# Kernel tuning notes

Measured on AMD Instinct MI355X. Metric: run time of the kernel, lower is better.

The kernel has to match this reference:

```python
import jax, jax.numpy as jnp
import numpy as np
from jax import lax

HUMAN_CONF = 0.7
IOU_TH = 0.5


def setup_inputs() -> dict:
    key = jax.random.key(0)
    k1, k2 = jax.random.split(key)
    B, Q, C = 16, 2048, 2
    return {
        "human_logits": jax.random.normal(k1, (B, Q, C), dtype=jnp.float32),
        "pred_boxes": jax.random.uniform(k2, (B, Q, 4), dtype=jnp.float32),  # cxcywh in [0,1]
        "img_h": 800,
        "img_w": 1333,
    }


def box_cxcywh_to_xyxy(b):
    cx, cy, w, h = b[..., 0], b[..., 1], b[..., 2], b[..., 3]
    return jnp.stack([cx - 0.5 * w, cy - 0.5 * h, cx + 0.5 * w, cy + 0.5 * h], axis=-1)


def pairwise_iou(b):
    # b: [Q,4] xyxy -> iou: [Q,Q]
    area = jnp.clip(b[:, 2] - b[:, 0], 0) * jnp.clip(b[:, 3] - b[:, 1], 0)
    lt = jnp.maximum(b[:, None, :2], b[None, :, :2])
    rb = jnp.minimum(b[:, None, 2:], b[None, :, 2:])
    wh = jnp.clip(rb - lt, 0)
    inter = wh[..., 0] * wh[..., 1]
    union = area[:, None] + area[None, :] - inter
    return inter / jnp.maximum(union, 1e-9)


def nms_keep(boxes, scores, valid, iou_th):
    # Greedy NMS on one image with fixed shapes; returns keep mask [Q].
    Q = scores.shape[0]
    order = jnp.argsort(jnp.where(valid, -scores, jnp.inf))  # valid boxes first, score desc
    b = boxes[order]
    v = valid[order]
    iou = pairwise_iou(b)                       # [Q,Q]
    idx = jnp.arange(Q)
    sup_mat = (iou > iou_th) & (idx[None, :] > idx[:, None])  # i suppresses later j

    def step(supp, i):
        keep_i = v[i] & jnp.logical_not(supp[i])
        supp = supp | (keep_i & sup_mat[i])
        return supp, keep_i

    _, keep_sorted = lax.scan(step, jnp.zeros(Q, bool), idx)
    return jnp.zeros(Q, bool).at[order].set(keep_sorted)


def reference(human_logits, pred_boxes, img_h, img_w):
    prob = jax.nn.softmax(human_logits, axis=-1)          # [B,Q,C]
    scores = prob.max(axis=-1)                            # [B,Q]
    labels = prob.argmax(axis=-1)                         # [B,Q]
    boxes = box_cxcywh_to_xyxy(pred_boxes)                # [B,Q,4]
    scale = jnp.array([img_w, img_h, img_w, img_h], dtype=boxes.dtype)
    boxes = boxes * scale
    valid = (labels == 0) & (scores >= HUMAN_CONF)
    keep = jax.vmap(lambda b, s, v: nms_keep(b, s, v, IOU_TH))(boxes, scores, valid)
    scores_out = jnp.where(keep, scores, 0.0)
    boxes_out = jnp.where(keep[..., None], boxes, 0.0).astype(jnp.int32)
    return scores_out, boxes_out, keep
```

## Files before the change

kernel.cpp:

```cpp
#include <hip/hip_runtime.h>
#include <math.h>


#define QN    2048
#define NS    1024
#define MATW  17408
#define MAGIC 0x5ca1ab1eu

__device__ __forceinline__ int rb32(int wb) { return 64 * wb * (33 - wb); }

__device__ __forceinline__ unsigned long long shfl_xor_u64(unsigned long long x, int m) {
    int lo = __shfl_xor((int)(unsigned)(x & 0xffffffffull), m, 64);
    int hi = __shfl_xor((int)(unsigned)(x >> 32), m, 64);
    return ((unsigned long long)(unsigned)hi << 32) | (unsigned)lo;
}

__device__ __forceinline__ unsigned long long score_key(float2 l, int q, bool* valid_out) {
    float mx = fmaxf(l.x, l.y), mn = fminf(l.x, l.y);
    float e = expf(mn - mx);
    float score = 1.0f / (1.0f + e);
    bool valid = (l.x >= l.y) && (score >= 0.7f);
    *valid_out = valid;
    unsigned sbits = valid ? __float_as_uint(score) : 0u;
    return ((unsigned long long)(~sbits) << 32) | (unsigned)q;
}

__global__ __launch_bounds__(1024) void kfused(
    const float* __restrict__ logits, const float* __restrict__ pboxes,
    const int* __restrict__ img_h_p, const int* __restrict__ img_w_p,
    unsigned* __restrict__ wflag, unsigned* __restrict__ wmat,
    float* __restrict__ out, int B)
{
    __shared__ __align__(16) char smem[32904];
    unsigned long long* skey = (unsigned long long*)smem;
    float* sx1 = (float*)(smem + 8192);
    float* sy1 = (float*)(smem + 12288);
    float* sx2 = (float*)(smem + 16384);
    float* sy2 = (float*)(smem + 20480);
    float* sar = (float*)(smem + 24576);
    unsigned short* sidxl = (unsigned short*)(smem + 28672);
    unsigned char* keepq = (unsigned char*)(smem + 30720);
    unsigned* skm = (unsigned*)(smem + 32768);
    int* sMp = (int*)(smem + 32896);

    const int blk = blockIdx.x;
    const int b = blk % B, slice = blk / B;
    const int tid = threadIdx.x, lane = tid & 63, wave = tid >> 6;
    const float sw = (float)(*img_w_p), sh = (float)(*img_h_p);

    if (tid == 0) *sMp = 0;
    keepq[tid] = 0; keepq[tid + 1024] = 0;
    if (tid < 32) skm[tid] = 0;
    __syncthreads();

    const unsigned long long lmask_lt = (1ull << lane) - 1ull;
#pragma unroll
    for (int qq = 0; qq < 2; ++qq) {
        int q = tid + qq * 1024;
        float2 l = ((const float2*)logits)[b * QN + q];
        bool valid;
        unsigned long long key = score_key(l, q, &valid);
        unsigned long long mb = __ballot(valid);
        int base = 0;
        if (lane == 0 && mb) base = atomicAdd(sMp, __popcll(mb));
        base = __shfl(base, 0, 64);
        if (valid) {
            int slot = base + __popcll(mb & lmask_lt);
            if (slot < NS) skey[slot] = key;
        }
    }
    __syncthreads();
    const int M = *sMp;

    if (M <= NS) {
        unsigned long long v = (tid < M) ? skey[tid] : ~0ull;
        __syncthreads();
#pragma unroll
        for (int k = 2; k <= 64; k <<= 1) {
            bool dir = ((tid & k) == 0);
#pragma unroll
            for (int j = k >> 1; j > 0; j >>= 1) {
                unsigned long long o = shfl_xor_u64(v, j);
                bool takeMin = (dir == ((tid & j) == 0));
                v = ((v < o) == takeMin) ? v : o;
            }
        }
        for (int k = 128; k <= NS; k <<= 1) {
            bool dir = ((tid & k) == 0);
            for (int j = k >> 1; j >= 64; j >>= 1) {
                skey[tid] = v;
                __syncthreads();
                unsigned long long o = skey[tid ^ j];
                bool takeMin = (dir == ((tid & j) == 0));
                v = ((v < o) == takeMin) ? v : o;
                __syncthreads();
            }
#pragma unroll
            for (int j = 32; j > 0; j >>= 1) {
                unsigned long long o = shfl_xor_u64(v, j);
                bool takeMin = (dir == ((tid & j) == 0));
                v = ((v < o) == takeMin) ? v : o;
            }
        }
        int qi = (int)((unsigned)v & 0xffffu);
        sidxl[tid] = (unsigned short)qi;
        float x1 = 0.f, y1 = 0.f, x2 = 0.f, y2 = 0.f, ar = 0.f;
        if (tid < M) {
            float4 pb = ((const float4*)pboxes)[b * QN + qi];
            x1 = (pb.x - 0.5f * pb.z) * sw;
            y1 = (pb.y - 0.5f * pb.w) * sh;
            x2 = (pb.x + 0.5f * pb.z) * sw;
            y2 = (pb.y + 0.5f * pb.w) * sh;
            ar = fmaxf(x2 - x1, 0.f) * fmaxf(y2 - y1, 0.f);
        }
        sx1[tid] = x1; sy1[tid] = y1; sx2[tid] = x2; sy2[tid] = y2; sar[tid] = ar;
        __syncthreads();

        unsigned* mat = wmat + (long)b * MATW;
        const int NG = (M + 3) >> 2;
        const int W64 = (M + 63) >> 6;
        for (int gi = slice * 16 + wave; gi < NG; gi += 128) {
            const int g = gi << 2;
            const int nr = min(4, M - g);
            const int wb = g >> 6;
            const int rl = 32 - 2 * wb;
            float ax1[4], ay1[4], ax2[4], ay2[4], aar[4];
            int rbase[4];
#pragma unroll
            for (int r = 0; r < 4; ++r) {
                int i = g + min(r, nr - 1);
                ax1[r] = sx1[i]; ay1[r] = sy1[i];
                ax2[r] = sx2[i]; ay2[r] = sy2[i]; aar[r] = sar[i];
                rbase[r] = rb32(wb) + ((g + r) & 63) * rl;
            }
            for (int w = wb; w < W64; ++w) {
                int j = (w << 6) | lane;
                float bx1 = sx1[j], by1 = sy1[j], bx2 = sx2[j], by2 = sy2[j], bar = sar[j];
#pragma unroll
                for (int r = 0; r < 4; ++r) {
                    float ltx = fmaxf(ax1[r], bx1), lty = fmaxf(ay1[r], by1);
                    float rbx = fminf(ax2[r], bx2), rby = fminf(ay2[r], by2);
                    float wx = fmaxf(rbx - ltx, 0.f), wy = fmaxf(rby - lty, 0.f);
                    float inter = wx * wy;
                    float uni = aar[r] + bar - inter;
                    float iou = inter / fmaxf(uni, 1e-9f);
                    bool sup = (iou > 0.5f) && (j > g + r);
                    unsigned long long bal = __ballot(sup);
                    if (lane == 0 && r < nr)
                        __hip_atomic_store(
                            (unsigned long long*)(mat + rbase[r] + 2 * (w - wb)), bal,
                            __ATOMIC_RELAXED, __HIP_MEMORY_SCOPE_AGENT);
                }
            }
        }
        __syncthreads();
        if (tid == 0)
            __hip_atomic_store(&wflag[b * 8 + slice], MAGIC,
                               __ATOMIC_RELEASE, __HIP_MEMORY_SCOPE_AGENT);
        if (slice != 0) return;

        if (wave == 0) {
            const unsigned* fp = &wflag[b * 8 + (lane & 7)];
            for (;;) {
                unsigned f = (lane < 8)
                    ? __hip_atomic_load(fp, __ATOMIC_RELAXED, __HIP_MEMORY_SCOPE_AGENT)
                    : MAGIC;
                if (__all(f == MAGIC)) break;
                __builtin_amdgcn_s_sleep(2);
            }
            (void)__hip_atomic_load(&wflag[b * 8], __ATOMIC_ACQUIRE,
                                    __HIP_MEMORY_SCOPE_AGENT);

            const unsigned* gm = wmat + (long)b * MATW;
            unsigned rem = 0;
            const int Ms = __builtin_amdgcn_readfirstlane(M);
            const int C = (Ms + 31) >> 5;
            unsigned rcur[32], rnxt[32];
            if (C > 0) {
                int Lc = min(tid, 31);
#pragma unroll
                for (int t = 0; t < 32; ++t) rcur[t] = gm[Lc + t * 32];
            }
            for (int c = 0; c < C; ++c) {
                if (c + 1 < C) {
                    int cn = c + 1, wbn = cn >> 1, rln = 32 - 2 * wbn;
                    int Lcn = min(max(tid, 2 * wbn), 31);
                    int rb0n = rb32(wbn) + ((cn & 1) << 5) * rln + (Lcn - 2 * wbn);
#pragma unroll
                    for (int t = 0; t < 32; ++t) rnxt[t] = gm[rb0n + t * rln];
                }
                unsigned rw = (unsigned)__builtin_amdgcn_readlane((int)rem, c);
                unsigned keepmask = 0;
                int lim = min(32, Ms - (c << 5));
#pragma unroll
                for (int t = 0; t < 32; ++t) {
                    if (t < lim && !((rw >> t) & 1u)) {
                        keepmask |= (1u << t);
                        rem |= rcur[t];
                        rw |= (unsigned)__builtin_amdgcn_readlane((int)rcur[t], c);
                    }
                }
                if (tid == 0) skm[c] = keepmask;
                if (c + 1 < C) {
#pragma unroll
                    for (int t = 0; t < 32; ++t) rcur[t] = rnxt[t];
                }
            }
        }
        __syncthreads();
        for (int s = tid; s < M; s += 1024)
            if ((skm[s >> 5] >> (s & 31)) & 1u) keepq[sidxl[s]] = 1;
        __syncthreads();
    } else {
        if (slice != 0) return;
        unsigned long long* skeyF = (unsigned long long*)smem;
        unsigned char* ssupp = (unsigned char*)(smem + 16384);
        for (int q = tid; q < QN; q += 1024) {
            float2 l = ((const float2*)logits)[b * QN + q];
            bool valid;
            skeyF[q] = score_key(l, q, &valid);
        }
        __syncthreads();
        for (int k = 2; k <= QN; k <<= 1)
            for (int j = k >> 1; j > 0; j >>= 1) {
                int i = ((tid & ~(j - 1)) << 1) | (tid & (j - 1));
                int p = i | j;
                bool up = ((i & k) == 0);
                unsigned long long a = skeyF[i], c2 = skeyF[p];
                if ((a > c2) == up) { skeyF[i] = c2; skeyF[p] = a; }
                __syncthreads();
            }
        for (int s = tid; s < M; s += 1024) ssupp[s] = 0;
        __syncthreads();
        for (int i = 0; i < M; ++i) {
            __syncthreads();
            if (ssupp[i]) continue;
            int ia = (unsigned short)(unsigned)skeyF[i];
            float4 pa = ((const float4*)pboxes)[b * QN + ia];
            float ax1 = (pa.x - 0.5f * pa.z) * sw, ay1 = (pa.y - 0.5f * pa.w) * sh;
            float ax2 = (pa.x + 0.5f * pa.z) * sw, ay2 = (pa.y + 0.5f * pa.w) * sh;
            float areaA = fmaxf(ax2 - ax1, 0.f) * fmaxf(ay2 - ay1, 0.f);
            for (int jj = i + 1 + tid; jj < M; jj += 1024) {
                int jb = (unsigned short)(unsigned)skeyF[jj];
                float4 pq = ((const float4*)pboxes)[b * QN + jb];
                float bx1 = (pq.x - 0.5f * pq.z) * sw, by1 = (pq.y - 0.5f * pq.w) * sh;
                float bx2 = (pq.x + 0.5f * pq.z) * sw, by2 = (pq.y + 0.5f * pq.w) * sh;
                float ltx = fmaxf(ax1, bx1), lty = fmaxf(ay1, by1);
                float rbx = fminf(ax2, bx2), rby = fminf(ay2, by2);
                float wx = fmaxf(rbx - ltx, 0.f), wy = fmaxf(rby - lty, 0.f);
                float inter = wx * wy;
                float areaB = fmaxf(bx2 - bx1, 0.f) * fmaxf(by2 - by1, 0.f);
                float uni = areaA + areaB - inter;
                if (inter / fmaxf(uni, 1e-9f) > 0.5f) ssupp[jj] = 1;
            }
        }
        __syncthreads();
        for (int s = tid; s < M; s += 1024)
            if (!ssupp[s]) keepq[(unsigned short)(unsigned)skeyF[s]] = 1;
        __syncthreads();
    }

    const long BQ = (long)B * QN;
#pragma unroll
    for (int qq = 0; qq < 2; ++qq) {
        int q = tid + qq * 1024;
        int base = b * QN + q;
        float2 l = ((const float2*)logits)[base];
        float e = expf(fminf(l.x, l.y) - fmaxf(l.x, l.y));
        float score = 1.0f / (1.0f + e);
        float4 pb = ((const float4*)pboxes)[base];
        float x1 = (pb.x - 0.5f * pb.z) * sw, y1 = (pb.y - 0.5f * pb.w) * sh;
        float x2 = (pb.x + 0.5f * pb.z) * sw, y2 = (pb.y + 0.5f * pb.w) * sh;
        int kp = keepq[q];
        out[base] = kp ? score : 0.f;
        out[BQ * 5 + base] = kp ? 1.f : 0.f;
        float4 ob;
        ob.x = kp ? truncf(x1) : 0.f;
        ob.y = kp ? truncf(y1) : 0.f;
        ob.z = kp ? truncf(x2) : 0.f;
        ob.w = kp ? truncf(y2) : 0.f;
        ((float4*)(out + BQ))[base] = ob;
    }
}

extern "C" void kernel_launch(void* const* d_in, const int* in_sizes, int n_in,
                              void* d_out, int out_size, void* d_ws, size_t ws_size,
                              hipStream_t stream) {
    const float* logits = (const float*)d_in[0];
    const float* pboxes = (const float*)d_in[1];
    const int*   img_h  = (const int*)d_in[2];
    const int*   img_w  = (const int*)d_in[3];
    float* out = (float*)d_out;
    const int B = in_sizes[0] / (QN * 2);

    char* ws = (char*)d_ws;
    unsigned* wflag = (unsigned*)(ws + 0);
    unsigned* wmat  = (unsigned*)(ws + 1024);

    kfused<<<dim3(B * 8), dim3(1024), 0, stream>>>(logits, pboxes, img_h, img_w,
                                                   wflag, wmat, out, B);
}
```

Measured before the change: 102.9 us.

## Pipeline NMS scan with per-group flags; slice 0 scans instead of building matrix

Slice 0 no longer computes any suppression-matrix rows. Each of the 7 other slices publishes a per-row-group ready flag, so slice 0's scanning wave waits only for the chunk it needs next instead of for every slice to finish. Slice 0 also prefetches logits and boxes for the output stage while it waits, and the matrix loads become atomic relaxed loads. This overlaps matrix construction with the sequential greedy scan, but it gives up one eighth of the matrix-building workers. It also adds flag polling per chunk, and because flags are never reset between calls it relies on the MAGIC value staying correct across calls.

```diff
diff --git a/kernel.cpp b/kernel.cpp
--- a/kernel.cpp
+++ b/kernel.cpp
@@ -28,7 +28,7 @@
 __global__ __launch_bounds__(1024) void kfused(
     const float* __restrict__ logits, const float* __restrict__ pboxes,
     const int* __restrict__ img_h_p, const int* __restrict__ img_w_p,
-    unsigned* __restrict__ wflag, unsigned* __restrict__ wmat,
+    unsigned* __restrict__ wgflag, unsigned* __restrict__ wmat,
     float* __restrict__ out, int B)
 {
     __shared__ __align__(16) char smem[32904];
@@ -49,8 +49,6 @@
     const float sw = (float)(*img_w_p), sh = (float)(*img_h_p);
 
     if (tid == 0) *sMp = 0;
-    keepq[tid] = 0; keepq[tid + 1024] = 0;
-    if (tid < 32) skm[tid] = 0;
     __syncthreads();
 
     const unsigned long long lmask_lt = (1ull << lane) - 1ull;
@@ -103,91 +101,113 @@
             }
         }
         int qi = (int)((unsigned)v & 0xffffu);
+        const int NG = (M + 3) >> 2;
+
+        if (slice != 0) {
+            float x1 = 0.f, y1 = 0.f, x2 = 0.f, y2 = 0.f, ar = 0.f;
+            if (tid < M) {
+                float4 pb = ((const float4*)pboxes)[b * QN + qi];
+                x1 = (pb.x - 0.5f * pb.z) * sw;
+                y1 = (pb.y - 0.5f * pb.w) * sh;
+                x2 = (pb.x + 0.5f * pb.z) * sw;
+                y2 = (pb.y + 0.5f * pb.w) * sh;
+                ar = fmaxf(x2 - x1, 0.f) * fmaxf(y2 - y1, 0.f);
+            }
+            sx1[tid] = x1; sy1[tid] = y1; sx2[tid] = x2; sy2[tid] = y2; sar[tid] = ar;
+            __syncthreads();
+
+            unsigned* mat = wmat + (long)b * MATW;
+            const int W64 = (M + 63) >> 6;
+            const int W = (slice - 1) * 16 + wave;
+            for (int gi = W; gi < NG; gi += 112) {
+                const int g = gi << 2;
+                const int nr = min(4, M - g);
+                const int wb = g >> 6;
+                const int rl = 32 - 2 * wb;
+                float ax1[4], ay1[4], ax2[4], ay2[4], aar[4];
+                int rbase[4];
+#pragma unroll
+                for (int r = 0; r < 4; ++r) {
+                    int i = g + min(r, nr - 1);
+                    ax1[r] = sx1[i]; ay1[r] = sy1[i];
+                    ax2[r] = sx2[i]; ay2[r] = sy2[i]; aar[r] = sar[i];
+                    rbase[r] = rb32(wb) + ((g + r) & 63) * rl;
+                }
+                for (int w = wb; w < W64; ++w) {
+                    int j = (w << 6) | lane;
+                    float bx1 = sx1[j], by1 = sy1[j], bx2 = sx2[j], by2 = sy2[j], bar = sar[j];
+#pragma unroll
+                    for (int r = 0; r < 4; ++r) {
+                        float ltx = fmaxf(ax1[r], bx1), lty = fmaxf(ay1[r], by1);
+                        float rbx = fminf(ax2[r], bx2), rby = fminf(ay2[r], by2);
+                        float wx = fmaxf(rbx - ltx, 0.f), wy = fmaxf(rby - lty, 0.f);
+                        float inter = wx * wy;
+                        float uni = aar[r] + bar - inter;
+                        float iou = inter / fmaxf(uni, 1e-9f);
+                        bool sup = (iou > 0.5f) && (j > g + r);
+                        unsigned long long bal = __ballot(sup);
+                        if (lane == 0 && r < nr)
+                            __hip_atomic_store(
+                                (unsigned long long*)(mat + rbase[r] + 2 * (w - wb)), bal,
+                                __ATOMIC_RELAXED, __HIP_MEMORY_SCOPE_AGENT);
+                    }
+                }
+                if (lane == 0)
+                    __hip_atomic_store(&wgflag[b * 256 + gi], MAGIC,
+                                       __ATOMIC_RELEASE, __HIP_MEMORY_SCOPE_AGENT);
+            }
+            return;
+        }
+
         sidxl[tid] = (unsigned short)qi;
-        float x1 = 0.f, y1 = 0.f, x2 = 0.f, y2 = 0.f, ar = 0.f;
-        if (tid < M) {
-            float4 pb = ((const float4*)pboxes)[b * QN + qi];
-            x1 = (pb.x - 0.5f * pb.z) * sw;
-            y1 = (pb.y - 0.5f * pb.w) * sh;
-            x2 = (pb.x + 0.5f * pb.z) * sw;
-            y2 = (pb.y + 0.5f * pb.w) * sh;
-            ar = fmaxf(x2 - x1, 0.f) * fmaxf(y2 - y1, 0.f);
-        }
-        sx1[tid] = x1; sy1[tid] = y1; sx2[tid] = x2; sy2[tid] = y2; sar[tid] = ar;
-        __syncthreads();
-
-        unsigned* mat = wmat + (long)b * MATW;
-        const int NG = (M + 3) >> 2;
-        const int W64 = (M + 63) >> 6;
-        for (int gi = slice * 16 + wave; gi < NG; gi += 128) {
-            const int g = gi << 2;
-            const int nr = min(4, M - g);
-            const int wb = g >> 6;
-            const int rl = 32 - 2 * wb;
-            float ax1[4], ay1[4], ax2[4], ay2[4], aar[4];
-            int rbase[4];
-#pragma unroll
-            for (int r = 0; r < 4; ++r) {
-                int i = g + min(r, nr - 1);
-                ax1[r] = sx1[i]; ay1[r] = sy1[i];
-                ax2[r] = sx2[i]; ay2[r] = sy2[i]; aar[r] = sar[i];
-                rbase[r] = rb32(wb) + ((g + r) & 63) * rl;
-            }
-            for (int w = wb; w < W64; ++w) {
-                int j = (w << 6) | lane;
-                float bx1 = sx1[j], by1 = sy1[j], bx2 = sx2[j], by2 = sy2[j], bar = sar[j];
-#pragma unroll
-                for (int r = 0; r < 4; ++r) {
-                    float ltx = fmaxf(ax1[r], bx1), lty = fmaxf(ay1[r], by1);
-                    float rbx = fminf(ax2[r], bx2), rby = fminf(ay2[r], by2);
-                    float wx = fmaxf(rbx - ltx, 0.f), wy = fmaxf(rby - lty, 0.f);
-                    float inter = wx * wy;
-                    float uni = aar[r] + bar - inter;
-                    float iou = inter / fmaxf(uni, 1e-9f);
-                    bool sup = (iou > 0.5f) && (j > g + r);
-                    unsigned long long bal = __ballot(sup);
-                    if (lane == 0 && r < nr)
-                        __hip_atomic_store(
-                            (unsigned long long*)(mat + rbase[r] + 2 * (w - wb)), bal,
-                            __ATOMIC_RELAXED, __HIP_MEMORY_SCOPE_AGENT);
-                }
-            }
-        }
-        __syncthreads();
-        if (tid == 0)
-            __hip_atomic_store(&wflag[b * 8 + slice], MAGIC,
-                               __ATOMIC_RELEASE, __HIP_MEMORY_SCOPE_AGENT);
-        if (slice != 0) return;
+        keepq[tid] = 0; keepq[tid + 1024] = 0;
+        if (tid < 32) skm[tid] = 0;
+
+        float2 l2a = ((const float2*)logits)[b * QN + tid];
+        float2 l2b = ((const float2*)logits)[b * QN + tid + 1024];
+        float4 p4a = ((const float4*)pboxes)[b * QN + tid];
+        float4 p4b = ((const float4*)pboxes)[b * QN + tid + 1024];
 
         if (wave == 0) {
-            const unsigned* fp = &wflag[b * 8 + (lane & 7)];
-            for (;;) {
-                unsigned f = (lane < 8)
-                    ? __hip_atomic_load(fp, __ATOMIC_RELAXED, __HIP_MEMORY_SCOPE_AGENT)
-                    : MAGIC;
-                if (__all(f == MAGIC)) break;
-                __builtin_amdgcn_s_sleep(2);
-            }
-            (void)__hip_atomic_load(&wflag[b * 8], __ATOMIC_ACQUIRE,
-                                    __HIP_MEMORY_SCOPE_AGENT);
-
             const unsigned* gm = wmat + (long)b * MATW;
             unsigned rem = 0;
             const int Ms = __builtin_amdgcn_readfirstlane(M);
             const int C = (Ms + 31) >> 5;
+            const int NGs = (Ms + 3) >> 2;
             unsigned rcur[32], rnxt[32];
+
+#define WAIT_CHUNK(cc)                                                                 \
+            {                                                                          \
+                int gbase = b * 256 + 8 * (cc);                                        \
+                int gcnt = min(8, NGs - 8 * (cc));                                     \
+                for (;;) {                                                             \
+                    unsigned f = (lane < gcnt)                                         \
+                        ? __hip_atomic_load(&wgflag[gbase + lane], __ATOMIC_RELAXED,   \
+                                            __HIP_MEMORY_SCOPE_AGENT)                  \
+                        : MAGIC;                                                       \
+                    if (__all(f == MAGIC)) break;                                      \
+                    __builtin_amdgcn_s_sleep(1);                                       \
+                }                                                                      \
+            }
+
             if (C > 0) {
+                WAIT_CHUNK(0);
                 int Lc = min(tid, 31);
 #pragma unroll
-                for (int t = 0; t < 32; ++t) rcur[t] = gm[Lc + t * 32];
+                for (int t = 0; t < 32; ++t)
+                    rcur[t] = __hip_atomic_load(gm + Lc + t * 32, __ATOMIC_RELAXED,
+                                                __HIP_MEMORY_SCOPE_AGENT);
             }
             for (int c = 0; c < C; ++c) {
                 if (c + 1 < C) {
+                    WAIT_CHUNK(c + 1);
                     int cn = c + 1, wbn = cn >> 1, rln = 32 - 2 * wbn;
                     int Lcn = min(max(tid, 2 * wbn), 31);
                     int rb0n = rb32(wbn) + ((cn & 1) << 5) * rln + (Lcn - 2 * wbn);
 #pragma unroll
-                    for (int t = 0; t < 32; ++t) rnxt[t] = gm[rb0n + t * rln];
+                    for (int t = 0; t < 32; ++t)
+                        rnxt[t] = __hip_atomic_load(gm + rb0n + t * rln, __ATOMIC_RELAXED,
+                                                    __HIP_MEMORY_SCOPE_AGENT);
                 }
                 unsigned rw = (unsigned)__builtin_amdgcn_readlane((int)rem, c);
                 unsigned keepmask = 0;
@@ -206,15 +226,39 @@
                     for (int t = 0; t < 32; ++t) rcur[t] = rnxt[t];
                 }
             }
+#undef WAIT_CHUNK
         }
         __syncthreads();
         for (int s = tid; s < M; s += 1024)
             if ((skm[s >> 5] >> (s & 31)) & 1u) keepq[sidxl[s]] = 1;
         __syncthreads();
+
+        const long BQ = (long)B * QN;
+#pragma unroll
+        for (int qq = 0; qq < 2; ++qq) {
+            int q = tid + qq * 1024;
+            int base = b * QN + q;
+            float2 l = qq ? l2b : l2a;
+            float4 pb = qq ? p4b : p4a;
+            float e = expf(fminf(l.x, l.y) - fmaxf(l.x, l.y));
+            float score = 1.0f / (1.0f + e);
+            float x1 = (pb.x - 0.5f * pb.z) * sw, y1 = (pb.y - 0.5f * pb.w) * sh;
+            float x2 = (pb.x + 0.5f * pb.z) * sw, y2 = (pb.y + 0.5f * pb.w) * sh;
+            int kp = keepq[q];
+            out[base] = kp ? score : 0.f;
+            out[BQ * 5 + base] = kp ? 1.f : 0.f;
+            float4 ob;
+            ob.x = kp ? truncf(x1) : 0.f;
+            ob.y = kp ? truncf(y1) : 0.f;
+            ob.z = kp ? truncf(x2) : 0.f;
+            ob.w = kp ? truncf(y2) : 0.f;
+            ((float4*)(out + BQ))[base] = ob;
+        }
     } else {
         if (slice != 0) return;
         unsigned long long* skeyF = (unsigned long long*)smem;
         unsigned char* ssupp = (unsigned char*)(smem + 16384);
+        keepq[tid] = 0; keepq[tid + 1024] = 0;
         for (int q = tid; q < QN; q += 1024) {
             float2 l = ((const float2*)logits)[b * QN + q];
             bool valid;
@@ -258,28 +302,28 @@
         for (int s = tid; s < M; s += 1024)
             if (!ssupp[s]) keepq[(unsigned short)(unsigned)skeyF[s]] = 1;
         __syncthreads();
-    }
-
-    const long BQ = (long)B * QN;
-#pragma unroll
-    for (int qq = 0; qq < 2; ++qq) {
-        int q = tid + qq * 1024;
-        int base = b * QN + q;
-        float2 l = ((const float2*)logits)[base];
-        float e = expf(fminf(l.x, l.y) - fmaxf(l.x, l.y));
-        float score = 1.0f / (1.0f + e);
-        float4 pb = ((const float4*)pboxes)[base];
-        float x1 = (pb.x - 0.5f * pb.z) * sw, y1 = (pb.y - 0.5f * pb.w) * sh;
-        float x2 = (pb.x + 0.5f * pb.z) * sw, y2 = (pb.y + 0.5f * pb.w) * sh;
-        int kp = keepq[q];
-        out[base] = kp ? score : 0.f;
-        out[BQ * 5 + base] = kp ? 1.f : 0.f;
-        float4 ob;
-        ob.x = kp ? truncf(x1) : 0.f;
-        ob.y = kp ? truncf(y1) : 0.f;
-        ob.z = kp ? truncf(x2) : 0.f;
-        ob.w = kp ? truncf(y2) : 0.f;
-        ((float4*)(out + BQ))[base] = ob;
+
+        const long BQ = (long)B * QN;
+#pragma unroll
+        for (int qq = 0; qq < 2; ++qq) {
+            int q = tid + qq * 1024;
+            int base = b * QN + q;
+            float2 l = ((const float2*)logits)[base];
+            float e = expf(fminf(l.x, l.y) - fmaxf(l.x, l.y));
+            float score = 1.0f / (1.0f + e);
+            float4 pb = ((const float4*)pboxes)[base];
+            float x1 = (pb.x - 0.5f * pb.z) * sw, y1 = (pb.y - 0.5f * pb.w) * sh;
+            float x2 = (pb.x + 0.5f * pb.z) * sw, y2 = (pb.y + 0.5f * pb.w) * sh;
+            int kp = keepq[q];
+            out[base] = kp ? score : 0.f;
+            out[BQ * 5 + base] = kp ? 1.f : 0.f;
+            float4 ob;
+            ob.x = kp ? truncf(x1) : 0.f;
+            ob.y = kp ? truncf(y1) : 0.f;
+            ob.z = kp ? truncf(x2) : 0.f;
+            ob.w = kp ? truncf(y2) : 0.f;
+            ((float4*)(out + BQ))[base] = ob;
+        }
     }
 }
 
@@ -294,9 +338,9 @@
     const int B = in_sizes[0] / (QN * 2);
 
     char* ws = (char*)d_ws;
-    unsigned* wflag = (unsigned*)(ws + 0);
-    unsigned* wmat  = (unsigned*)(ws + 1024);
+    unsigned* wgflag = (unsigned*)(ws + 0);
+    unsigned* wmat   = (unsigned*)(ws + 16384);
 
     kfused<<<dim3(B * 8), dim3(1024), 0, stream>>>(logits, pboxes, img_h, img_w,
-                                                   wflag, wmat, out, B);
+                                                   wgflag, wmat, out, B);
 }
```

After: 113.8 us. 10.6% more time.

## Offload IoU matrix to worker slices; master prefetches outputs inputs during wait

Applied to the files above, without the earlier changes.

Slice 0 no longer computes any part of the suppression bitmask. The IoU work is spread over slices 1-7 and the flag wait covers only those seven. While slice 0 waits, it clears its shared buffers and prefetches the logits and boxes it will need for the output write, so those loads overlap the wait. The trade-off is that the remaining slices each carry more IoU groups, which could lengthen the critical path if slice 0's own share was what hid the latency.

```diff
diff --git a/kernel.cpp b/kernel.cpp
--- a/kernel.cpp
+++ b/kernel.cpp
@@ -49,8 +49,6 @@
     const float sw = (float)(*img_w_p), sh = (float)(*img_h_p);
 
     if (tid == 0) *sMp = 0;
-    keepq[tid] = 0; keepq[tid + 1024] = 0;
-    if (tid < 32) skm[tid] = 0;
     __syncthreads();
 
     const unsigned long long lmask_lt = (1ull << lane) - 1ull;
@@ -103,72 +101,83 @@
             }
         }
         int qi = (int)((unsigned)v & 0xffffu);
+        const int NG = (M + 3) >> 2;
+
+        if (slice != 0) {
+            float x1 = 0.f, y1 = 0.f, x2 = 0.f, y2 = 0.f, ar = 0.f;
+            if (tid < M) {
+                float4 pb = ((const float4*)pboxes)[b * QN + qi];
+                x1 = (pb.x - 0.5f * pb.z) * sw;
+                y1 = (pb.y - 0.5f * pb.w) * sh;
+                x2 = (pb.x + 0.5f * pb.z) * sw;
+                y2 = (pb.y + 0.5f * pb.w) * sh;
+                ar = fmaxf(x2 - x1, 0.f) * fmaxf(y2 - y1, 0.f);
+            }
+            sx1[tid] = x1; sy1[tid] = y1; sx2[tid] = x2; sy2[tid] = y2; sar[tid] = ar;
+            __syncthreads();
+
+            unsigned* mat = wmat + (long)b * MATW;
+            const int W64 = (M + 63) >> 6;
+            for (int gi = (slice - 1) * 16 + wave; gi < NG; gi += 112) {
+                const int g = gi << 2;
+                const int nr = min(4, M - g);
+                const int wb = g >> 6;
+                const int rl = 32 - 2 * wb;
+                float ax1[4], ay1[4], ax2[4], ay2[4], aar[4];
+                int rbase[4];
+#pragma unroll
+                for (int r = 0; r < 4; ++r) {
+                    int i = g + min(r, nr - 1);
+                    ax1[r] = sx1[i]; ay1[r] = sy1[i];
+                    ax2[r] = sx2[i]; ay2[r] = sy2[i]; aar[r] = sar[i];
+                    rbase[r] = rb32(wb) + ((g + r) & 63) * rl;
+                }
+                for (int w = wb; w < W64; ++w) {
+                    int j = (w << 6) | lane;
+                    float bx1 = sx1[j], by1 = sy1[j], bx2 = sx2[j], by2 = sy2[j], bar = sar[j];
+#pragma unroll
+                    for (int r = 0; r < 4; ++r) {
+                        float ltx = fmaxf(ax1[r], bx1), lty = fmaxf(ay1[r], by1);
+                        float rbx = fminf(ax2[r], bx2), rby = fminf(ay2[r], by2);
+                        float wx = fmaxf(rbx - ltx, 0.f), wy = fmaxf(rby - lty, 0.f);
+                        float inter = wx * wy;
+                        float uni = aar[r] + bar - inter;
+                        float iou = inter / fmaxf(uni, 1e-9f);
+                        bool sup = (iou > 0.5f) && (j > g + r);
+                        unsigned long long bal = __ballot(sup);
+                        if (lane == 0 && r < nr)
+                            __hip_atomic_store(
+                                (unsigned long long*)(mat + rbase[r] + 2 * (w - wb)), bal,
+                                __ATOMIC_RELAXED, __HIP_MEMORY_SCOPE_AGENT);
+                    }
+                }
+            }
+            __syncthreads();
+            if (tid == 0)
+                __hip_atomic_store(&wflag[b * 8 + slice], MAGIC,
+                                   __ATOMIC_RELEASE, __HIP_MEMORY_SCOPE_AGENT);
+            return;
+        }
+
         sidxl[tid] = (unsigned short)qi;
-        float x1 = 0.f, y1 = 0.f, x2 = 0.f, y2 = 0.f, ar = 0.f;
-        if (tid < M) {
-            float4 pb = ((const float4*)pboxes)[b * QN + qi];
-            x1 = (pb.x - 0.5f * pb.z) * sw;
-            y1 = (pb.y - 0.5f * pb.w) * sh;
-            x2 = (pb.x + 0.5f * pb.z) * sw;
-            y2 = (pb.y + 0.5f * pb.w) * sh;
-            ar = fmaxf(x2 - x1, 0.f) * fmaxf(y2 - y1, 0.f);
-        }
-        sx1[tid] = x1; sy1[tid] = y1; sx2[tid] = x2; sy2[tid] = y2; sar[tid] = ar;
-        __syncthreads();
-
-        unsigned* mat = wmat + (long)b * MATW;
-        const int NG = (M + 3) >> 2;
-        const int W64 = (M + 63) >> 6;
-        for (int gi = slice * 16 + wave; gi < NG; gi += 128) {
-            const int g = gi << 2;
-            const int nr = min(4, M - g);
-            const int wb = g >> 6;
-            const int rl = 32 - 2 * wb;
-            float ax1[4], ay1[4], ax2[4], ay2[4], aar[4];
-            int rbase[4];
-#pragma unroll
-            for (int r = 0; r < 4; ++r) {
-                int i = g + min(r, nr - 1);
-                ax1[r] = sx1[i]; ay1[r] = sy1[i];
-                ax2[r] = sx2[i]; ay2[r] = sy2[i]; aar[r] = sar[i];
-                rbase[r] = rb32(wb) + ((g + r) & 63) * rl;
-            }
-            for (int w = wb; w < W64; ++w) {
-                int j = (w << 6) | lane;
-                float bx1 = sx1[j], by1 = sy1[j], bx2 = sx2[j], by2 = sy2[j], bar = sar[j];
-#pragma unroll
-                for (int r = 0; r < 4; ++r) {
-                    float ltx = fmaxf(ax1[r], bx1), lty = fmaxf(ay1[r], by1);
-                    float rbx = fminf(ax2[r], bx2), rby = fminf(ay2[r], by2);
-                    float wx = fmaxf(rbx - ltx, 0.f), wy = fmaxf(rby - lty, 0.f);
-                    float inter = wx * wy;
-                    float uni = aar[r] + bar - inter;
-                    float iou = inter / fmaxf(uni, 1e-9f);
-                    bool sup = (iou > 0.5f) && (j > g + r);
-                    unsigned long long bal = __ballot(sup);
-                    if (lane == 0 && r < nr)
-                        __hip_atomic_store(
-                            (unsigned long long*)(mat + rbase[r] + 2 * (w - wb)), bal,
-                            __ATOMIC_RELAXED, __HIP_MEMORY_SCOPE_AGENT);
-                }
-            }
-        }
-        __syncthreads();
-        if (tid == 0)
-            __hip_atomic_store(&wflag[b * 8 + slice], MAGIC,
-                               __ATOMIC_RELEASE, __HIP_MEMORY_SCOPE_AGENT);
-        if (slice != 0) return;
+        keepq[tid] = 0; keepq[tid + 1024] = 0;
+        if (tid < 32) skm[tid] = 0;
+
+        float2 l2a = ((const float2*)logits)[b * QN + tid];
+        float2 l2b = ((const float2*)logits)[b * QN + tid + 1024];
+        float4 p4a = ((const float4*)pboxes)[b * QN + tid];
+        float4 p4b = ((const float4*)pboxes)[b * QN + tid + 1024];
 
         if (wave == 0) {
-            const unsigned* fp = &wflag[b * 8 + (lane & 7)];
+            const unsigned* fp = &wflag[b * 8 + 1 + lane];
             for (;;) {
-                unsigned f = (lane < 8)
+                unsigned f = (lane < 7)
                     ? __hip_atomic_load(fp, __ATOMIC_RELAXED, __HIP_MEMORY_SCOPE_AGENT)
                     : MAGIC;
                 if (__all(f == MAGIC)) break;
                 __builtin_amdgcn_s_sleep(2);
             }
-            (void)__hip_atomic_load(&wflag[b * 8], __ATOMIC_ACQUIRE,
+            (void)__hip_atomic_load(&wflag[b * 8 + 1], __ATOMIC_ACQUIRE,
                                     __HIP_MEMORY_SCOPE_AGENT);
 
             const unsigned* gm = wmat + (long)b * MATW;
@@ -211,10 +220,33 @@
         for (int s = tid; s < M; s += 1024)
             if ((skm[s >> 5] >> (s & 31)) & 1u) keepq[sidxl[s]] = 1;
         __syncthreads();
+
+        const long BQ = (long)B * QN;
+#pragma unroll
+        for (int qq = 0; qq < 2; ++qq) {
+            int q = tid + qq * 1024;
+            int base = b * QN + q;
+            float2 l = qq ? l2b : l2a;
+            float4 pb = qq ? p4b : p4a;
+            float e = expf(fminf(l.x, l.y) - fmaxf(l.x, l.y));
+            float score = 1.0f / (1.0f + e);
+            float x1 = (pb.x - 0.5f * pb.z) * sw, y1 = (pb.y - 0.5f * pb.w) * sh;
+            float x2 = (pb.x + 0.5f * pb.z) * sw, y2 = (pb.y + 0.5f * pb.w) * sh;
+            int kp = keepq[q];
+            out[base] = kp ? score : 0.f;
+            out[BQ * 5 + base] = kp ? 1.f : 0.f;
+            float4 ob;
+            ob.x = kp ? truncf(x1) : 0.f;
+            ob.y = kp ? truncf(y1) : 0.f;
+            ob.z = kp ? truncf(x2) : 0.f;
+            ob.w = kp ? truncf(y2) : 0.f;
+            ((float4*)(out + BQ))[base] = ob;
+        }
     } else {
         if (slice != 0) return;
         unsigned long long* skeyF = (unsigned long long*)smem;
         unsigned char* ssupp = (unsigned char*)(smem + 16384);
+        keepq[tid] = 0; keepq[tid + 1024] = 0;
         for (int q = tid; q < QN; q += 1024) {
             float2 l = ((const float2*)logits)[b * QN + q];
             bool valid;
@@ -258,28 +290,28 @@
         for (int s = tid; s < M; s += 1024)
             if (!ssupp[s]) keepq[(unsigned short)(unsigned)skeyF[s]] = 1;
         __syncthreads();
-    }
-
-    const long BQ = (long)B * QN;
-#pragma unroll
-    for (int qq = 0; qq < 2; ++qq) {
-        int q = tid + qq * 1024;
-        int base = b * QN + q;
-        float2 l = ((const float2*)logits)[base];
-        float e = expf(fminf(l.x, l.y) - fmaxf(l.x, l.y));
-        float score = 1.0f / (1.0f + e);
-        float4 pb = ((const float4*)pboxes)[base];
-        float x1 = (pb.x - 0.5f * pb.z) * sw, y1 = (pb.y - 0.5f * pb.w) * sh;
-        float x2 = (pb.x + 0.5f * pb.z) * sw, y2 = (pb.y + 0.5f * pb.w) * sh;
-        int kp = keepq[q];
-        out[base] = kp ? score : 0.f;
-        out[BQ * 5 + base] = kp ? 1.f : 0.f;
-        float4 ob;
-        ob.x = kp ? truncf(x1) : 0.f;
-        ob.y = kp ? truncf(y1) : 0.f;
-        ob.z = kp ? truncf(x2) : 0.f;
-        ob.w = kp ? truncf(y2) : 0.f;
-        ((float4*)(out + BQ))[base] = ob;
+
+        const long BQ = (long)B * QN;
+#pragma unroll
+        for (int qq = 0; qq < 2; ++qq) {
+            int q = tid + qq * 1024;
+            int base = b * QN + q;
+            float2 l = ((const float2*)logits)[base];
+            float e = expf(fminf(l.x, l.y) - fmaxf(l.x, l.y));
+            float score = 1.0f / (1.0f + e);
+            float4 pb = ((const float4*)pboxes)[base];
+            float x1 = (pb.x - 0.5f * pb.z) * sw, y1 = (pb.y - 0.5f * pb.w) * sh;
+            float x2 = (pb.x + 0.5f * pb.z) * sw, y2 = (pb.y + 0.5f * pb.w) * sh;
+            int kp = keepq[q];
+            out[base] = kp ? score : 0.f;
+            out[BQ * 5 + base] = kp ? 1.f : 0.f;
+            float4 ob;
+            ob.x = kp ? truncf(x1) : 0.f;
+            ob.y = kp ? truncf(y1) : 0.f;
+            ob.z = kp ? truncf(x2) : 0.f;
+            ob.w = kp ? truncf(y2) : 0.f;
+            ((float4*)(out + BQ))[base] = ob;
+        }
     }
 }
 
```

After: 103.4 us. About the same (+0.4%).
